# Kernel optimization log

Measured on AMD Instinct MI355X. Metric: run time of the kernel, lower is better.

## Reference

```python
import jax, jax.numpy as jnp
import numpy as np


def setup_inputs() -> dict:
    key = jax.random.key(0)
    kq, kk, kv = jax.random.split(key, 3)
    B, H, S, D = 2, 16, 2048, 64
    Q = jax.random.normal(kq, (B, H, S, D), dtype=jnp.float32)
    K = jax.random.normal(kk, (B, 1, S, D), dtype=jnp.float32)
    V = jax.random.normal(kv, (B, 1, S, D), dtype=jnp.float32)
    return {"Q": Q, "K": K, "V": V}


def reference(Q, K, V):
    # Multi-query attention: K/V have a single head broadcast over Q's heads.
    head_dim = Q.shape[-1]
    scale = 1.0 / (head_dim ** 0.5)
    k = K[:, 0]  # [B, S, D]
    v = V[:, 0]  # [B, S, D]
    # scores[b,h,i,j] = Q[b,h,i] . K[b,j] * scale
    scores = jnp.einsum("bhid,bjd->bhij", Q, k) * scale
    attn = jax.nn.softmax(scores, axis=-1)
    out = jnp.einsum("bhij,bjd->bhid", attn, v)
    return out
```

## Files before the change

kernel.cpp:

```cpp
#include <hip/hip_runtime.h>
#include <hip/hip_bf16.h>

typedef __attribute__((ext_vector_type(8))) short bf16x8;
typedef __attribute__((ext_vector_type(4))) short bf16x4;
typedef __attribute__((ext_vector_type(16))) float f32x16;
typedef unsigned short u16;
typedef unsigned int u32;

#define S_LEN 2048
#define HD 64

__device__ __forceinline__ u16 f2bf(float x) {
  __hip_bfloat16 h = __float2bfloat16(x);
  return __builtin_bit_cast(u16, h);
}

__device__ __forceinline__ u32 pk2(float lo, float hi) {
  return ((u32)f2bf(hi) << 16) | (u32)f2bf(lo);
}

__device__ __forceinline__ int swz(int idx) {
  return idx ^ (((idx >> 6) & 7) << 3);
}

__device__ __forceinline__ void gload16(const u16* g, u16* lds) {
  __builtin_amdgcn_global_load_lds(
      (const __attribute__((address_space(1))) u32*)g,
      (__attribute__((address_space(3))) u32*)lds, 16, 0, 0);
}

#if __has_builtin(__builtin_amdgcn_mfma_f32_32x32x8bf16_1k)
__device__ __forceinline__ f32x16 mfma8(bf16x4 a, bf16x4 b, f32x16 c) {
  return __builtin_amdgcn_mfma_f32_32x32x8bf16_1k(a, b, c, 0, 0, 0);
}
#else
__device__ __forceinline__ f32x16 mfma8(bf16x4 a, bf16x4 b, f32x16 c) {
  asm volatile("v_mfma_f32_32x32x8_bf16 %0, %1, %2, %0\n\ts_nop 7\n\ts_nop 7"
               : "+v"(c) : "v"(a), "v"(b));
  return c;
}
#endif

__global__ void prep(const float* __restrict__ K, const float* __restrict__ V,
                     u16* __restrict__ Kb, u16* __restrict__ VTb) {
  int i = blockIdx.x * 256 + threadIdx.x;
  if (i < 65536) {
    float4 v = reinterpret_cast<const float4*>(K)[i];
    ushort4 o;
    o.x = f2bf(v.x); o.y = f2bf(v.y); o.z = f2bf(v.z); o.w = f2bf(v.w);
    reinterpret_cast<ushort4*>(Kb)[i] = o;
  } else {
    int j = i - 65536;
    int kv = j & (S_LEN - 1);
    int r = j >> 11;
    int d = r & 63;
    int b = r >> 6;
    VTb[j] = f2bf(V[((size_t)(b * S_LEN + kv)) * HD + d]);
  }
}

__launch_bounds__(256, 2)
__global__ void attn_fwd(const float* __restrict__ Q, const u16* __restrict__ Kb,
                         const u16* __restrict__ VTb, float* __restrict__ out) {
  __shared__ u16 Kt[2][64 * 64];
  __shared__ u16 VTt[2][64 * 64];

  const int tid = threadIdx.x;
  const int w = tid >> 6;
  const int lane = tid & 63;
  const int q = lane & 31;
  const int hi = lane >> 5;

  const int bh = blockIdx.x >> 4;
  const int qt = blockIdx.x & 15;
  const int b = bh >> 4;
  const int q0w = qt * 128 + w * 32;

  const u16* Kbase = Kb + (size_t)b * S_LEN * HD;
  const u16* Vbase = VTb + (size_t)b * HD * S_LEN;

  const int sr = lane >> 3;
  const int cs = (lane & 7) ^ sr;

  const float qs = 0.125f * 1.44269504f;
  bf16x8 qreg[4];
  {
    const float* qrow = Q + ((size_t)(bh * S_LEN + q0w + q)) * HD + 8 * hi;
    #pragma unroll
    for (int s = 0; s < 4; ++s) {
      float4 f0 = *reinterpret_cast<const float4*>(qrow + 16 * s);
      float4 f1 = *reinterpret_cast<const float4*>(qrow + 16 * s + 4);
      bf16x8 v;
      v[0] = f2bf(f0.x * qs); v[1] = f2bf(f0.y * qs);
      v[2] = f2bf(f0.z * qs); v[3] = f2bf(f0.w * qs);
      v[4] = f2bf(f1.x * qs); v[5] = f2bf(f1.y * qs);
      v[6] = f2bf(f1.z * qs); v[7] = f2bf(f1.w * qs);
      qreg[s] = v;
    }
  }

  f32x16 oacc0, oacc1;
  #pragma unroll
  for (int i = 0; i < 16; ++i) { oacc0[i] = 0.f; oacc1[i] = 0.f; }
  float m = -1e30f, l = 0.f;

  #pragma unroll
  for (int h = 0; h < 2; ++h) {
    int row = h * 32 + w * 8 + sr;
    gload16(Kbase + (size_t)row * HD + cs * 8, &Kt[0][h * 2048 + w * 512]);
    gload16(Vbase + (size_t)row * S_LEN + cs * 8, &VTt[0][h * 2048 + w * 512]);
  }
  __syncthreads();

  int cur = 0;
  for (int t = 0; t < 32; ++t) {
    if (t != 31) {
      int kv1 = (t + 1) * 64;
      #pragma unroll
      for (int h = 0; h < 2; ++h) {
        int row = h * 32 + w * 8 + sr;
        gload16(Kbase + (size_t)(kv1 + row) * HD + cs * 8,
                &Kt[cur ^ 1][h * 2048 + w * 512]);
        gload16(Vbase + (size_t)row * S_LEN + kv1 + cs * 8,
                &VTt[cur ^ 1][h * 2048 + w * 512]);
      }
    }

    f32x16 s0, s1;
    #pragma unroll
    for (int i = 0; i < 16; ++i) { s0[i] = 0.f; s1[i] = 0.f; }
    __builtin_amdgcn_s_setprio(1);
    #pragma unroll
    for (int s = 0; s < 4; ++s) {
      bf16x8 k0 = *reinterpret_cast<const bf16x8*>(&Kt[cur][swz(q * 64 + 16 * s + 8 * hi)]);
      bf16x8 k1 = *reinterpret_cast<const bf16x8*>(&Kt[cur][swz((32 + q) * 64 + 16 * s + 8 * hi)]);
      s0 = __builtin_amdgcn_mfma_f32_32x32x16_bf16(k0, qreg[s], s0, 0, 0, 0);
      s1 = __builtin_amdgcn_mfma_f32_32x32x16_bf16(k1, qreg[s], s1, 0, 0, 0);
    }
    __builtin_amdgcn_s_setprio(0);

    float pm = s0[0];
    #pragma unroll
    for (int i = 1; i < 16; ++i) pm = fmaxf(pm, s0[i]);
    #pragma unroll
    for (int i = 0; i < 16; ++i) pm = fmaxf(pm, s1[i]);
    pm = fmaxf(pm, __shfl_xor(pm, 32));

    if (__any(pm > m + 8.f)) {
      float mn = fmaxf(m, pm);
      float corr = exp2f(m - mn);
      m = mn;
      l *= corr;
      #pragma unroll
      for (int r = 0; r < 16; ++r) {
        int qr = (r & 3) + 8 * (r >> 2) + 4 * hi;
        float cr = __shfl(corr, qr);
        oacc0[r] *= cr;
        oacc1[r] *= cr;
      }
    }

    float p0[16], p1[16];
    float la = 0.f;
    #pragma unroll
    for (int i = 0; i < 16; ++i) { p0[i] = exp2f(s0[i] - m); la += p0[i]; }
    #pragma unroll
    for (int i = 0; i < 16; ++i) { p1[i] = exp2f(s1[i] - m); la += p1[i]; }
    l += la;

    union PW { u32 w[2]; bf16x4 v; };
    __builtin_amdgcn_s_setprio(1);
    #pragma unroll
    for (int t8 = 0; t8 < 8; ++t8) {
      PW pa;
      if (t8 < 4) {
        pa.w[0] = pk2(p0[4 * t8], p0[4 * t8 + 1]);
        pa.w[1] = pk2(p0[4 * t8 + 2], p0[4 * t8 + 3]);
      } else {
        int u = 4 * (t8 - 4);
        pa.w[0] = pk2(p1[u], p1[u + 1]);
        pa.w[1] = pk2(p1[u + 2], p1[u + 3]);
      }
      bf16x4 v0 = *reinterpret_cast<const bf16x4*>(&VTt[cur][swz(q * 64 + 8 * t8 + 4 * hi)]);
      bf16x4 v1 = *reinterpret_cast<const bf16x4*>(&VTt[cur][swz((32 + q) * 64 + 8 * t8 + 4 * hi)]);
      oacc0 = mfma8(pa.v, v0, oacc0);
      oacc1 = mfma8(pa.v, v1, oacc1);
    }
    __builtin_amdgcn_s_setprio(0);

    __syncthreads();
    cur ^= 1;
  }

  float lt = l + __shfl_xor(l, 32);
  float invq = 1.0f / lt;
  #pragma unroll
  for (int r = 0; r < 16; ++r) {
    int qr = (r & 3) + 8 * (r >> 2) + 4 * hi;
    float iv = __shfl(invq, qr);
    size_t o = ((size_t)(bh * S_LEN + q0w + qr)) * HD + q;
    out[o] = oacc0[r] * iv;
    out[o + 32] = oacc1[r] * iv;
  }
}

extern "C" void kernel_launch(void* const* d_in, const int* in_sizes, int n_in,
                              void* d_out, int out_size, void* d_ws, size_t ws_size,
                              hipStream_t stream) {
  const float* Q = (const float*)d_in[0];
  const float* K = (const float*)d_in[1];
  const float* V = (const float*)d_in[2];
  float* out = (float*)d_out;

  const int KN = 2 * S_LEN * HD;
  u16* Kb = (u16*)d_ws;
  u16* VTb = Kb + KN;

  hipLaunchKernelGGL(prep, dim3((65536 + KN) / 256), dim3(256), 0, stream,
                     K, V, Kb, VTb);
  hipLaunchKernelGGL(attn_fwd, dim3(512), dim3(256), 0, stream, Q, Kb, VTb, out);
}
```

Measured before the change: 140.1 us.

## Fold running max into MFMA init, permute V layout for wide LDS reads

Seeds the QK^T MFMA accumulator with -m, so scores arrive already shifted and the per-element subtraction before exp2 goes away. The max update now runs only on a rarely taken threshold branch. V^T is stored with a permuted key order so each lane can read 16 bytes from LDS instead of two 8-byte reads. P is packed to bf16 with the hardware v_cvt_pk_bf16_f32 instruction, and the max and sum reductions are split into four chains to increase ILP. The permuted layout must stay exactly in step with the MFMA operand mapping, and carrying the max in the accumulator can change rounding slightly.

```diff
diff --git a/kernel.cpp b/kernel.cpp
--- a/kernel.cpp
+++ b/kernel.cpp
@@ -15,8 +15,10 @@
   return __builtin_bit_cast(u16, h);
 }
 
-__device__ __forceinline__ u32 pk2(float lo, float hi) {
-  return ((u32)f2bf(hi) << 16) | (u32)f2bf(lo);
+__device__ __forceinline__ u32 cvtpk(float lo, float hi) {
+  u32 r;
+  asm("v_cvt_pk_bf16_f32 %0, %1, %2" : "=v"(r) : "v"(lo), "v"(hi));
+  return r;
 }
 
 __device__ __forceinline__ int swz(int idx) {
@@ -51,11 +53,14 @@
     reinterpret_cast<ushort4*>(Kb)[i] = o;
   } else {
     int j = i - 65536;
-    int kv = j & (S_LEN - 1);
+    int kv2 = j & (S_LEN - 1);
     int r = j >> 11;
     int d = r & 63;
     int b = r >> 6;
-    VTb[j] = f2bf(V[((size_t)(b * S_LEN + kv)) * HD + d]);
+    int g = (kv2 >> 2) & 3;
+    int gs = ((g & 1) << 1) | (g >> 1);
+    int kvs = (kv2 & ~15) | (gs << 2) | (kv2 & 3);
+    VTb[j] = f2bf(V[((size_t)(b * S_LEN + kvs)) * HD + d]);
   }
 }
 
@@ -99,10 +104,10 @@
     }
   }
 
-  f32x16 oacc0, oacc1;
+  f32x16 oacc0, oacc1, minit;
   #pragma unroll
-  for (int i = 0; i < 16; ++i) { oacc0[i] = 0.f; oacc1[i] = 0.f; }
-  float m = -1e30f, l = 0.f;
+  for (int i = 0; i < 16; ++i) { oacc0[i] = 0.f; oacc1[i] = 0.f; minit[i] = 0.f; }
+  float m = 0.f, l = 0.f;
 
   #pragma unroll
   for (int h = 0; h < 2; ++h) {
@@ -126,12 +131,13 @@
       }
     }
 
-    f32x16 s0, s1;
-    #pragma unroll
-    for (int i = 0; i < 16; ++i) { s0[i] = 0.f; s1[i] = 0.f; }
     __builtin_amdgcn_s_setprio(1);
-    #pragma unroll
-    for (int s = 0; s < 4; ++s) {
+    bf16x8 ka0 = *reinterpret_cast<const bf16x8*>(&Kt[cur][swz(q * 64 + 8 * hi)]);
+    bf16x8 ka1 = *reinterpret_cast<const bf16x8*>(&Kt[cur][swz((32 + q) * 64 + 8 * hi)]);
+    f32x16 s0 = __builtin_amdgcn_mfma_f32_32x32x16_bf16(ka0, qreg[0], minit, 0, 0, 0);
+    f32x16 s1 = __builtin_amdgcn_mfma_f32_32x32x16_bf16(ka1, qreg[0], minit, 0, 0, 0);
+    #pragma unroll
+    for (int s = 1; s < 4; ++s) {
       bf16x8 k0 = *reinterpret_cast<const bf16x8*>(&Kt[cur][swz(q * 64 + 16 * s + 8 * hi)]);
       bf16x8 k1 = *reinterpret_cast<const bf16x8*>(&Kt[cur][swz((32 + q) * 64 + 16 * s + 8 * hi)]);
       s0 = __builtin_amdgcn_mfma_f32_32x32x16_bf16(k0, qreg[s], s0, 0, 0, 0);
@@ -139,18 +145,28 @@
     }
     __builtin_amdgcn_s_setprio(0);
 
-    float pm = s0[0];
-    #pragma unroll
-    for (int i = 1; i < 16; ++i) pm = fmaxf(pm, s0[i]);
-    #pragma unroll
-    for (int i = 0; i < 16; ++i) pm = fmaxf(pm, s1[i]);
+    float ma = s0[0], mb = s0[1], mc = s0[2], md = s0[3];
+    #pragma unroll
+    for (int i = 4; i < 16; i += 4) {
+      ma = fmaxf(ma, s0[i]);     mb = fmaxf(mb, s0[i + 1]);
+      mc = fmaxf(mc, s0[i + 2]); md = fmaxf(md, s0[i + 3]);
+    }
+    #pragma unroll
+    for (int i = 0; i < 16; i += 4) {
+      ma = fmaxf(ma, s1[i]);     mb = fmaxf(mb, s1[i + 1]);
+      mc = fmaxf(mc, s1[i + 2]); md = fmaxf(md, s1[i + 3]);
+    }
+    float pm = fmaxf(fmaxf(ma, mb), fmaxf(mc, md));
     pm = fmaxf(pm, __shfl_xor(pm, 32));
 
-    if (__any(pm > m + 8.f)) {
-      float mn = fmaxf(m, pm);
-      float corr = exp2f(m - mn);
-      m = mn;
+    float p0v[16], p1v[16];
+    if (__builtin_expect(__any(pm > 8.f), 0)) {
+      float delta = fmaxf(pm, 0.f);
+      float corr = exp2f(-delta);
+      m += delta;
       l *= corr;
+      #pragma unroll
+      for (int i = 0; i < 16; ++i) minit[i] = -m;
       #pragma unroll
       for (int r = 0; r < 16; ++r) {
         int qr = (r & 3) + 8 * (r >> 2) + 4 * hi;
@@ -158,33 +174,55 @@
         oacc0[r] *= cr;
         oacc1[r] *= cr;
       }
-    }
-
-    float p0[16], p1[16];
-    float la = 0.f;
-    #pragma unroll
-    for (int i = 0; i < 16; ++i) { p0[i] = exp2f(s0[i] - m); la += p0[i]; }
-    #pragma unroll
-    for (int i = 0; i < 16; ++i) { p1[i] = exp2f(s1[i] - m); la += p1[i]; }
-    l += la;
-
-    union PW { u32 w[2]; bf16x4 v; };
+      #pragma unroll
+      for (int i = 0; i < 16; ++i) p0v[i] = exp2f(s0[i] - delta);
+      #pragma unroll
+      for (int i = 0; i < 16; ++i) p1v[i] = exp2f(s1[i] - delta);
+    } else {
+      #pragma unroll
+      for (int i = 0; i < 16; ++i) p0v[i] = exp2f(s0[i]);
+      #pragma unroll
+      for (int i = 0; i < 16; ++i) p1v[i] = exp2f(s1[i]);
+    }
+
+    {
+      float sa_ = p0v[0], sb_ = p0v[1], sc_ = p0v[2], sd_ = p0v[3];
+      #pragma unroll
+      for (int i = 4; i < 16; i += 4) {
+        sa_ += p0v[i];     sb_ += p0v[i + 1];
+        sc_ += p0v[i + 2]; sd_ += p0v[i + 3];
+      }
+      #pragma unroll
+      for (int i = 0; i < 16; i += 4) {
+        sa_ += p1v[i];     sb_ += p1v[i + 1];
+        sc_ += p1v[i + 2]; sd_ += p1v[i + 3];
+      }
+      l += (sa_ + sb_) + (sc_ + sd_);
+    }
+
+    u32 pw[16];
+    #pragma unroll
+    for (int k = 0; k < 8; ++k) pw[k] = cvtpk(p0v[2 * k], p0v[2 * k + 1]);
+    #pragma unroll
+    for (int k = 0; k < 8; ++k) pw[8 + k] = cvtpk(p1v[2 * k], p1v[2 * k + 1]);
+
+    union PW2 { u32 w[2]; bf16x4 v; };
     __builtin_amdgcn_s_setprio(1);
     #pragma unroll
-    for (int t8 = 0; t8 < 8; ++t8) {
-      PW pa;
-      if (t8 < 4) {
-        pa.w[0] = pk2(p0[4 * t8], p0[4 * t8 + 1]);
-        pa.w[1] = pk2(p0[4 * t8 + 2], p0[4 * t8 + 3]);
-      } else {
-        int u = 4 * (t8 - 4);
-        pa.w[0] = pk2(p1[u], p1[u + 1]);
-        pa.w[1] = pk2(p1[u + 2], p1[u + 3]);
-      }
-      bf16x4 v0 = *reinterpret_cast<const bf16x4*>(&VTt[cur][swz(q * 64 + 8 * t8 + 4 * hi)]);
-      bf16x4 v1 = *reinterpret_cast<const bf16x4*>(&VTt[cur][swz((32 + q) * 64 + 8 * t8 + 4 * hi)]);
-      oacc0 = mfma8(pa.v, v0, oacc0);
-      oacc1 = mfma8(pa.v, v1, oacc1);
+    for (int tp = 0; tp < 4; ++tp) {
+      bf16x8 vv0 = *reinterpret_cast<const bf16x8*>(&VTt[cur][swz(q * 64 + 16 * tp + 8 * hi)]);
+      bf16x8 vv1 = *reinterpret_cast<const bf16x8*>(&VTt[cur][swz((32 + q) * 64 + 16 * tp + 8 * hi)]);
+      bf16x4 vl0 = __builtin_shufflevector(vv0, vv0, 0, 1, 2, 3);
+      bf16x4 vh0 = __builtin_shufflevector(vv0, vv0, 4, 5, 6, 7);
+      bf16x4 vl1 = __builtin_shufflevector(vv1, vv1, 0, 1, 2, 3);
+      bf16x4 vh1 = __builtin_shufflevector(vv1, vv1, 4, 5, 6, 7);
+      PW2 pa, pb;
+      pa.w[0] = pw[4 * tp + 0]; pa.w[1] = pw[4 * tp + 1];
+      pb.w[0] = pw[4 * tp + 2]; pb.w[1] = pw[4 * tp + 3];
+      oacc0 = mfma8(pa.v, vl0, oacc0);
+      oacc0 = mfma8(pb.v, vh0, oacc0);
+      oacc1 = mfma8(pa.v, vl1, oacc1);
+      oacc1 = mfma8(pb.v, vh1, oacc1);
     }
     __builtin_amdgcn_s_setprio(0);
 
```

After: 145.8 us. +4.1%, slower.

## Split KV range across two wave groups per block with LDS merge

Applied to the files above, without the earlier changes.

Doubles the block to 512 threads: two groups of four waves each process half of the KV sequence for the same 128 query rows. Their partial softmax states are then merged through LDS at the end. The change aims to raise occupancy and latency hiding, since there are only 512 blocks on many CUs. It also permutes V columns in prep so the PV MFMAs can use 8-wide LDS reads. It also switches to the native exp2 builtin and hoists the bf16 packing of P. The costs are a final merge pass, higher LDS use, a changed initial max (m=0 instead of -1e30), and reliance on the permutation matching the MFMA operand layout.

```diff
diff --git a/kernel.cpp b/kernel.cpp
--- a/kernel.cpp
+++ b/kernel.cpp
@@ -9,6 +9,12 @@
 
 #define S_LEN 2048
 #define HD 64
+
+#if __has_builtin(__builtin_amdgcn_exp2f)
+#define EXP2(x) __builtin_amdgcn_exp2f(x)
+#else
+#define EXP2(x) exp2f(x)
+#endif
 
 __device__ __forceinline__ u16 f2bf(float x) {
   __hip_bfloat16 h = __float2bfloat16(x);
@@ -51,22 +57,26 @@
     reinterpret_cast<ushort4*>(Kb)[i] = o;
   } else {
     int j = i - 65536;
-    int kv = j & (S_LEN - 1);
+    int kv2 = j & (S_LEN - 1);
     int r = j >> 11;
     int d = r & 63;
     int b = r >> 6;
-    VTb[j] = f2bf(V[((size_t)(b * S_LEN + kv)) * HD + d]);
-  }
-}
-
-__launch_bounds__(256, 2)
+    int g = (kv2 >> 2) & 3;
+    int gs = ((g & 1) << 1) | (g >> 1);
+    int kvs = (kv2 & ~15) | (gs << 2) | (kv2 & 3);
+    VTb[j] = f2bf(V[((size_t)(b * S_LEN + kvs)) * HD + d]);
+  }
+}
+
+__launch_bounds__(512, 4)
 __global__ void attn_fwd(const float* __restrict__ Q, const u16* __restrict__ Kb,
                          const u16* __restrict__ VTb, float* __restrict__ out) {
-  __shared__ u16 Kt[2][64 * 64];
-  __shared__ u16 VTt[2][64 * 64];
+  __shared__ __align__(16) u16 smem[32768];
 
   const int tid = threadIdx.x;
   const int w = tid >> 6;
+  const int wq = w & 3;
+  const int half = w >> 2;
   const int lane = tid & 63;
   const int q = lane & 31;
   const int hi = lane >> 5;
@@ -74,7 +84,7 @@
   const int bh = blockIdx.x >> 4;
   const int qt = blockIdx.x & 15;
   const int b = bh >> 4;
-  const int q0w = qt * 128 + w * 32;
+  const int q0w = qt * 128 + wq * 32;
 
   const u16* Kbase = Kb + (size_t)b * S_LEN * HD;
   const u16* Vbase = VTb + (size_t)b * HD * S_LEN;
@@ -102,29 +112,37 @@
   f32x16 oacc0, oacc1;
   #pragma unroll
   for (int i = 0; i < 16; ++i) { oacc0[i] = 0.f; oacc1[i] = 0.f; }
-  float m = -1e30f, l = 0.f;
-
-  #pragma unroll
-  for (int h = 0; h < 2; ++h) {
-    int row = h * 32 + w * 8 + sr;
-    gload16(Kbase + (size_t)row * HD + cs * 8, &Kt[0][h * 2048 + w * 512]);
-    gload16(Vbase + (size_t)row * S_LEN + cs * 8, &VTt[0][h * 2048 + w * 512]);
+  float m = 0.f, l = 0.f;
+
+  {
+    int kv0 = half * 1024;
+    u16* T = &smem[half * 8192];
+    #pragma unroll
+    for (int hh = 0; hh < 2; ++hh) {
+      int r0 = wq * 16 + hh * 8;
+      int row = r0 + sr;
+      gload16(Kbase + (size_t)(kv0 + row) * HD + cs * 8, T + r0 * 64);
+      gload16(Vbase + (size_t)row * S_LEN + kv0 + cs * 8, T + 4096 + r0 * 64);
+    }
   }
   __syncthreads();
 
   int cur = 0;
-  for (int t = 0; t < 32; ++t) {
-    if (t != 31) {
-      int kv1 = (t + 1) * 64;
+  for (int t = 0; t < 16; ++t) {
+    if (t != 15) {
+      int kv1 = (half * 16 + t + 1) * 64;
+      u16* T = &smem[((cur ^ 1) * 2 + half) * 8192];
       #pragma unroll
-      for (int h = 0; h < 2; ++h) {
-        int row = h * 32 + w * 8 + sr;
-        gload16(Kbase + (size_t)(kv1 + row) * HD + cs * 8,
-                &Kt[cur ^ 1][h * 2048 + w * 512]);
-        gload16(Vbase + (size_t)row * S_LEN + kv1 + cs * 8,
-                &VTt[cur ^ 1][h * 2048 + w * 512]);
+      for (int hh = 0; hh < 2; ++hh) {
+        int r0 = wq * 16 + hh * 8;
+        int row = r0 + sr;
+        gload16(Kbase + (size_t)(kv1 + row) * HD + cs * 8, T + r0 * 64);
+        gload16(Vbase + (size_t)row * S_LEN + kv1 + cs * 8, T + 4096 + r0 * 64);
       }
     }
+
+    const u16* Kt = &smem[(cur * 2 + half) * 8192];
+    const u16* VTt = Kt + 4096;
 
     f32x16 s0, s1;
     #pragma unroll
@@ -132,8 +150,8 @@
     __builtin_amdgcn_s_setprio(1);
     #pragma unroll
     for (int s = 0; s < 4; ++s) {
-      bf16x8 k0 = *reinterpret_cast<const bf16x8*>(&Kt[cur][swz(q * 64 + 16 * s + 8 * hi)]);
-      bf16x8 k1 = *reinterpret_cast<const bf16x8*>(&Kt[cur][swz((32 + q) * 64 + 16 * s + 8 * hi)]);
+      bf16x8 k0 = *reinterpret_cast<const bf16x8*>(&Kt[swz(q * 64 + 16 * s + 8 * hi)]);
+      bf16x8 k1 = *reinterpret_cast<const bf16x8*>(&Kt[swz((32 + q) * 64 + 16 * s + 8 * hi)]);
       s0 = __builtin_amdgcn_mfma_f32_32x32x16_bf16(k0, qreg[s], s0, 0, 0, 0);
       s1 = __builtin_amdgcn_mfma_f32_32x32x16_bf16(k1, qreg[s], s1, 0, 0, 0);
     }
@@ -148,7 +166,7 @@
 
     if (__any(pm > m + 8.f)) {
       float mn = fmaxf(m, pm);
-      float corr = exp2f(m - mn);
+      float corr = EXP2(m - mn);
       m = mn;
       l *= corr;
       #pragma unroll
@@ -160,31 +178,37 @@
       }
     }
 
-    float p0[16], p1[16];
+    float p0v[16], p1v[16];
     float la = 0.f;
     #pragma unroll
-    for (int i = 0; i < 16; ++i) { p0[i] = exp2f(s0[i] - m); la += p0[i]; }
-    #pragma unroll
-    for (int i = 0; i < 16; ++i) { p1[i] = exp2f(s1[i] - m); la += p1[i]; }
+    for (int i = 0; i < 16; ++i) { p0v[i] = EXP2(s0[i] - m); la += p0v[i]; }
+    #pragma unroll
+    for (int i = 0; i < 16; ++i) { p1v[i] = EXP2(s1[i] - m); la += p1v[i]; }
     l += la;
 
-    union PW { u32 w[2]; bf16x4 v; };
+    u32 pw[16];
+    #pragma unroll
+    for (int k = 0; k < 8; ++k) pw[k] = pk2(p0v[2 * k], p0v[2 * k + 1]);
+    #pragma unroll
+    for (int k = 0; k < 8; ++k) pw[8 + k] = pk2(p1v[2 * k], p1v[2 * k + 1]);
+
+    union PW2 { u32 w[2]; bf16x4 v; };
     __builtin_amdgcn_s_setprio(1);
     #pragma unroll
-    for (int t8 = 0; t8 < 8; ++t8) {
-      PW pa;
-      if (t8 < 4) {
-        pa.w[0] = pk2(p0[4 * t8], p0[4 * t8 + 1]);
-        pa.w[1] = pk2(p0[4 * t8 + 2], p0[4 * t8 + 3]);
-      } else {
-        int u = 4 * (t8 - 4);
-        pa.w[0] = pk2(p1[u], p1[u + 1]);
-        pa.w[1] = pk2(p1[u + 2], p1[u + 3]);
-      }
-      bf16x4 v0 = *reinterpret_cast<const bf16x4*>(&VTt[cur][swz(q * 64 + 8 * t8 + 4 * hi)]);
-      bf16x4 v1 = *reinterpret_cast<const bf16x4*>(&VTt[cur][swz((32 + q) * 64 + 8 * t8 + 4 * hi)]);
-      oacc0 = mfma8(pa.v, v0, oacc0);
-      oacc1 = mfma8(pa.v, v1, oacc1);
+    for (int tp = 0; tp < 4; ++tp) {
+      bf16x8 vv0 = *reinterpret_cast<const bf16x8*>(&VTt[swz(q * 64 + 16 * tp + 8 * hi)]);
+      bf16x8 vv1 = *reinterpret_cast<const bf16x8*>(&VTt[swz((32 + q) * 64 + 16 * tp + 8 * hi)]);
+      bf16x4 vl0 = __builtin_shufflevector(vv0, vv0, 0, 1, 2, 3);
+      bf16x4 vh0 = __builtin_shufflevector(vv0, vv0, 4, 5, 6, 7);
+      bf16x4 vl1 = __builtin_shufflevector(vv1, vv1, 0, 1, 2, 3);
+      bf16x4 vh1 = __builtin_shufflevector(vv1, vv1, 4, 5, 6, 7);
+      PW2 pa, pb;
+      pa.w[0] = pw[4 * tp + 0]; pa.w[1] = pw[4 * tp + 1];
+      pb.w[0] = pw[4 * tp + 2]; pb.w[1] = pw[4 * tp + 3];
+      oacc0 = mfma8(pa.v, vl0, oacc0);
+      oacc0 = mfma8(pb.v, vh0, oacc0);
+      oacc1 = mfma8(pa.v, vl1, oacc1);
+      oacc1 = mfma8(pb.v, vh1, oacc1);
     }
     __builtin_amdgcn_s_setprio(0);
 
@@ -193,14 +217,36 @@
   }
 
   float lt = l + __shfl_xor(l, 32);
-  float invq = 1.0f / lt;
-  #pragma unroll
-  for (int r = 0; r < 16; ++r) {
-    int qr = (r & 3) + 8 * (r >> 2) + 4 * hi;
-    float iv = __shfl(invq, qr);
-    size_t o = ((size_t)(bh * S_LEN + q0w + qr)) * HD + q;
-    out[o] = oacc0[r] * iv;
-    out[o + 32] = oacc1[r] * iv;
+  float* fO = (float*)smem;
+  float* fL = fO + 8192;
+  float* fM = fL + 128;
+
+  if (half == 1) {
+    #pragma unroll
+    for (int r = 0; r < 16; ++r) {
+      fO[(wq * 32 + r) * 64 + lane] = oacc0[r];
+      fO[(wq * 32 + 16 + r) * 64 + lane] = oacc1[r];
+    }
+    if (hi == 0) { fL[wq * 32 + q] = lt; fM[wq * 32 + q] = m; }
+  }
+  __syncthreads();
+  if (half == 0) {
+    #pragma unroll
+    for (int r = 0; r < 16; ++r) {
+      int qr = (r & 3) + 8 * (r >> 2) + 4 * hi;
+      float mA = __shfl(m, qr);
+      float lA = __shfl(lt, qr);
+      float mB = fM[wq * 32 + qr];
+      float lB = fL[wq * 32 + qr];
+      float M = fmaxf(mA, mB);
+      float ca = EXP2(mA - M), cb = EXP2(mB - M);
+      float iv = 1.0f / (ca * lA + cb * lB);
+      float ob0 = fO[(wq * 32 + r) * 64 + lane];
+      float ob1 = fO[(wq * 32 + 16 + r) * 64 + lane];
+      size_t o = ((size_t)(bh * S_LEN + q0w + qr)) * HD + q;
+      out[o]      = (ca * oacc0[r] + cb * ob0) * iv;
+      out[o + 32] = (ca * oacc1[r] + cb * ob1) * iv;
+    }
   }
 }
 
@@ -218,5 +264,5 @@
 
   hipLaunchKernelGGL(prep, dim3((65536 + KN) / 256), dim3(256), 0, stream,
                      K, V, Kb, VTb);
-  hipLaunchKernelGGL(attn_fwd, dim3(512), dim3(256), 0, stream, Q, Kb, VTb, out);
-}
+  hipLaunchKernelGGL(attn_fwd, dim3(512), dim3(512), 0, stream, Q, Kb, VTb, out);
+}
```

Result: faster. 127.0 us (-9.3%).
